# Performance work log

Hardware: AMD Instinct MI355X
Metric: run time of the kernel (lower is better)

The kernel has to match this reference:

```python
import jax, jax.numpy as jnp
import numpy as np

G, N, E, B, L, D, R, NB, H, LD = 5, 50000, 250000, 50, 200, 64, 5, 2, 4, 32
NU, NV = 100000, 50000
NE = NU + NV  # embedding rows


def _rgcn(x, src, dst, etype, basis, comp, root, bias):
    # basis-decomposed RGCN layer with per-(node,relation) mean aggregation
    xb = jnp.einsum('ni,bio->nbo', x, basis)              # [N,NB,out]
    msg = jnp.einsum('eb,ebo->eo', comp[etype], xb[src])  # [E,out]
    seg = dst * R + etype                                  # (node,relation) segment id
    agg = jax.ops.segment_sum(msg, seg, num_segments=N * R)
    cnt = jax.ops.segment_sum(jnp.ones_like(msg[:, 0]), seg, num_segments=N * R)
    agg = agg / jnp.maximum(cnt, 1.0)[:, None]
    return agg.reshape(N, R, -1).sum(1) + x @ root + bias


def _stam(inp, pos_emb, Qw, Kw, Vw, convW, convb):
    Bn = inp.shape[0]
    t = inp + pos_emb[None]                                # [2B,L,D]
    def heads(m):
        return (t @ m).reshape(Bn, L, H, D // H).transpose(0, 2, 1, 3)
    q, k, v = heads(Qw), heads(Kw), heads(Vw)
    scores = jnp.einsum('bhld,bhmd->bhlm', q, k) / np.float32(np.sqrt(L))
    att = jax.nn.softmax(scores, axis=-1)                  # mask is all-ones -> adder 0
    h = jnp.einsum('bhlm,bhmd->bhld', att, v).transpose(0, 2, 1, 3).reshape(Bn, L, D)
    ff = jnp.einsum('ol,bld->bod', convW, h) + convb[None, :, None] + h  # Conv1d k=1 over the L-channel axis + residual
    out = t + ff
    return out / jnp.maximum(jnp.linalg.norm(out, axis=2, keepdims=True), 1e-12)


def _forward(x, temporal_label, emb_table, basis0, comp0, root0, bias0,
             basisR, compR, rootR, biasR, pos_emb, Qw, Kw, Vw, convW, convb,
             aw1, ab1, aw2, mw1, mb1, mw2, mb2, l1w, l1b, l2w, l2b,
             edge_index, edge_type, centre_index, temporal_table):
    x_list, tem_list = [], []
    for g in range(G):
        xg = x[g]
        src, dst, et = edge_index[g, 0], edge_index[g, 1], edge_type[g]
        h = jnp.tanh(_rgcn(xg, src, dst, et, basis0, comp0, root0, bias0))
        states = [h]
        for l in range(3):
            h = jnp.tanh(_rgcn(h, src, dst, et, basisR[l], compR[l], rootR[l], biasR[l]))
            states.append(h)
        cs = jnp.concatenate(states, 1)                    # [N,128]
        u_idx = jnp.nonzero(xg[:, 0] == 1, size=B, fill_value=0)[0]
        i_idx = jnp.nonzero(xg[:, 1] == 1, size=B, fill_value=0)[0]
        x_list.append(jnp.concatenate([cs[u_idx], cs[i_idx]], 1))  # [B,256]
        tem_in = emb_table[temporal_table[g]]              # [2B,L,D]
        tem_out = _stam(tem_in, pos_emb, Qw, Kw, Vw, convW, convb)
        W1 = emb_table[centre_index[g]]                    # [2B,D]
        tw = jax.nn.softmax(jnp.einsum('btd,bd->bt', tem_out, W1), axis=1)
        am = tw * temporal_label[g]
        asum = am / jnp.sum(am, axis=1, keepdims=True)
        asum = jnp.where(jnp.isfinite(asum), asum, 0.0)
        _emb = jnp.einsum('bt,btd->bd', asum, tem_in)      # sparse mm equivalent
        tem_list.append(_emb.reshape(B, -1))               # [B,128]
    graph_tem = jnp.concatenate(tem_list, 1)               # [B,640]
    graph_emb = jnp.concatenate(x_list, 1)                 # [B,1280]
    sub = jnp.stack(x_list, 1)                             # [B,G,256]
    attK = jax.nn.relu(sub @ aw1 + ab1) @ aw2              # [B,G,1]
    attw = jax.nn.softmax(attK, axis=1)
    agg = jnp.sum(attw * sub, axis=1)                      # [B,256]
    meta = jax.nn.relu(agg @ mw1 + mb1) @ mw2 + mb2        # [B,1280]
    xcat = jnp.concatenate([meta * graph_emb, graph_tem], 1)  # [B,1920]
    hh = jax.nn.relu(xcat @ l1w + l1b)
    return (hh @ l2w + l2b)[:, 0]


def setup_inputs():
    key = jax.random.key(0)
    ks = jax.random.split(key, 32)
    cls = np.full((G, N), 2, dtype=np.int64)
    cls[:, :B] = 0          # users
    cls[:, B:2 * B] = 1     # items
    cls[:, 2 * B::2] = 3    # mix of 1-hop neighbor classes
    x = jax.nn.one_hot(jnp.asarray(cls), 4, dtype=jnp.float32)
    def nrm(k, shape, s=0.1):
        return jax.random.normal(k, shape, jnp.float32) * s
    return dict(
        x=x,
        edge_index=jax.random.randint(ks[0], (G, 2, E), 0, N),
        edge_type=jax.random.randint(ks[1], (G, E), 0, R),
        centre_index=jax.random.randint(ks[2], (G, 2 * B), 0, NE),
        temporal_table=jax.random.randint(ks[3], (G, 2 * B, L), 0, NE),
        temporal_label=(jax.random.uniform(ks[4], (G, 2 * B, L)) < 0.5).astype(jnp.float32),
        emb_table=nrm(ks[5], (NE, D), 0.01),
        basis0=nrm(ks[6], (NB, 4, LD)), comp0=nrm(ks[7], (R, NB), 1.0),
        root0=nrm(ks[8], (4, LD)), bias0=jnp.zeros((LD,), jnp.float32),
        basisR=nrm(ks[9], (3, NB, LD, LD)), compR=nrm(ks[10], (3, R, NB), 1.0),
        rootR=nrm(ks[11], (3, LD, LD)), biasR=jnp.zeros((3, LD), jnp.float32),
        pos_emb=nrm(ks[12], (L, D), 0.01),
        Qw=nrm(ks[13], (D, D), 0.01), Kw=nrm(ks[14], (D, D), 0.01), Vw=nrm(ks[15], (D, D), 0.01),
        convW=nrm(ks[16], (L, L), 0.05), convb=jnp.zeros((L,), jnp.float32),
        aw1=nrm(ks[17], (8 * LD, 8 * LD), 0.05), ab1=jnp.zeros((8 * LD,), jnp.float32),
        aw2=nrm(ks[18], (8 * LD, 1), 0.05),
        mw1=nrm(ks[19], (8 * LD, 16 * LD), 0.05), mb1=jnp.zeros((16 * LD,), jnp.float32),
        mw2=nrm(ks[20], (16 * LD, G * 8 * LD), 0.05), mb2=jnp.zeros((G * 8 * LD,), jnp.float32),
        l1w=nrm(ks[21], (G * 2 * D + G * 8 * LD, 128), 0.05), l1b=jnp.zeros((128,), jnp.float32),
        l2w=nrm(ks[22], (128, 1), 0.05), l2b=jnp.zeros((1,), jnp.float32),
    )


def reference(x, temporal_label, emb_table, basis0, comp0, root0, bias0,
              basisR, compR, rootR, biasR, pos_emb, Qw, Kw, Vw, convW, convb,
              aw1, ab1, aw2, mw1, mb1, mw2, mb2, l1w, l1b, l2w, l2b,
              edge_index, edge_type, centre_index, temporal_table):
    return _forward(x, temporal_label, emb_table, basis0, comp0, root0, bias0,
                    basisR, compR, rootR, biasR, pos_emb, Qw, Kw, Vw, convW, convb,
                    aw1, ab1, aw2, mw1, mb1, mw2, mb2, l1w, l1b, l2w, l2b,
                    edge_index, edge_type, centre_index, temporal_table)
```

## Files before the change

### kernel.cpp

```cpp
#include <hip/hip_runtime.h>
#include <hip/hip_bf16.h>

__global__ void IGMC_15247133901635_kernel() {}

#define cG 5
#define cN 50000
#define cE 250000
#define cB 50
#define cL 200
#define cD 64
#define cR 5
#define cNR 250000
#define cGB 500
#define NBLK 977

#define FP_UIDX   0
#define FP_BSUM   4096
#define FP_XLIST  28672
#define FP_EMBOUT 540672
#define FP_ATTK   668672
#define FP_METAH  672768
#define FP_XCAT   775168
#define FP_SAG    1159168
#define FP_INV    1559168
#define FP_CLS    2559168
#define FP_HA     3559168
#define FP_HB     9959168
#define FP_CUR    16359168
#define FP_OFF    21359168
#define FP_PERM   26359168
#define FP_INVC   31359168
#define FP_NEED   36359168ULL
#define FP2_MARK   36359168
#define FP2_LIST   37359168
#define FP2_CNT    38359168
#define FP2_COUNTS 38363264
#define FP2_NEED   38367360ULL

__global__ void k_prep(const float* xg, int* cls, int* cur) {
  int i = blockIdx.x * 256 + threadIdx.x;
  if (i < cNR) cur[i] = 0;
  if (i < cN) {
    int c = 0;
    if (xg[i * 4 + 1] == 1.0f) c = 1;
    else if (xg[i * 4 + 2] == 1.0f) c = 2;
    else if (xg[i * 4 + 3] == 1.0f) c = 3;
    cls[i] = c;
  }
}

__global__ void k_histg(const int* eid, const int* etg, int* cur) {
  int e = blockIdx.x * 256 + threadIdx.x;
  if (e < cE) atomicAdd(&cur[eid[e] * cR + etg[e]], 1);
}

__global__ void k_bsum(const int* cur, int* bsum) {
  __shared__ int sC[256];
  int t = threadIdx.x;
  int i = blockIdx.x * 256 + t;
  sC[t] = (i < cNR) ? cur[i] : 0;
  __syncthreads();
  for (int s = 128; s > 0; s >>= 1) {
    if (t < s) sC[t] += sC[t + s];
    __syncthreads();
  }
  if (t == 0) bsum[blockIdx.x] = sC[0];
}

__global__ void __launch_bounds__(1024) k_bscan(int* bsum) {
  __shared__ int sS[1024];
  int t = threadIdx.x;
  int v = (t < NBLK) ? bsum[t] : 0;
  sS[t] = v;
  __syncthreads();
  for (int off = 1; off < 1024; off <<= 1) {
    int add = (t >= off) ? sS[t - off] : 0;
    __syncthreads();
    sS[t] += add;
    __syncthreads();
  }
  if (t < NBLK) bsum[t] = sS[t] - v;
}

__global__ void k_mkoff(int* cur, int* off, const int* bbase) {
  __shared__ int sC[256];
  __shared__ int sO[256];
  int t = threadIdx.x;
  int i = blockIdx.x * 256 + t;
  int c = (i < cNR) ? cur[i] : 0;
  sC[t] = c;
  __syncthreads();
  if (t == 0) {
    int run = 0;
    for (int k = 0; k < 256; k++) { sO[k] = run; run += sC[k]; }
  }
  __syncthreads();
  if (i < cNR) {
    int v = bbase[blockIdx.x] + sO[t];
    off[i] = v;
    cur[i] = v;
  }
}

__global__ void k_scatter(const int* eis, const int* eid, const int* etg,
                          const int* cls, int* cur, int* perm) {
  int e = blockIdx.x * 256 + threadIdx.x;
  if (e >= cE) return;
  int src = eis[e];
  int r = etg[e];
  int bin = eid[e] * cR + r;
  int pos = atomicAdd(&cur[bin], 1);
  perm[pos] = src * 32 + r * 4 + cls[src];
}

__global__ void k_invc(const int* off, const int* cur, float* invc) {
  int i = blockIdx.x * 256 + threadIdx.x;
  if (i >= cNR) return;
  int st = off[i], en = cur[i];
  if (en > st) {
    float ic = 1.0f / (float)(en - st);
// ... 189 lines not shown
  for (; j + 1 < en; j += 2) {
    int p0 = perm[j], p1 = perm[j + 1];
    float i0 = invc[j], i1 = invc[j + 1];
    tot += sW0[(p0 & 31) * 32 + li] * i0 + sW0[(p1 & 31) * 32 + li] * i1;
  }
  if (j < en) tot += sW0[(perm[j] & 31) * 32 + li] * invc[j];
  float val = tanhf(tot + sRt[cls[n] * 32 + li] + sB[li]);
  hout[(long long)n * 32 + li] = val;
  if (inv) {
    int iv = inv[n];
    if (iv >= 0) xlist[iv + li] = val;
  }
}

__global__ void k_gatherR(const int* off, const int* cur, const int* perm,
                          const float* invc, const float* hin, const float* basis,
                          const float* comp, const float* root, const float* bias,
                          float* hout, const int* inv, float* xlist, int layer,
                          const int* list, const int* cntp) {
  int cnt = cN;
  if (cntp) {
    cnt = *cntp;
    if (blockIdx.x * 8 >= cnt) return;
  }
  __shared__ float sB0[1024];
  __shared__ float sB1[1024];
  __shared__ float sRt[1024];
  __shared__ float sZ0[8][32];
  __shared__ float sZ1[8][32];
  __shared__ float sHl[8][32];
  __shared__ float sBias[32];
  __shared__ float sC0[8];
  __shared__ float sC1[8];
  int t = threadIdx.x;
  for (int idx = t; idx < 1024; idx += 256) {
    sB0[idx] = basis[idx];
    sB1[idx] = basis[1024 + idx];
    sRt[idx] = root[idx];
  }
  if (t < 32) sBias[t] = bias[t];
  if (t < cR) { sC0[t] = comp[t * 2]; sC1[t] = comp[t * 2 + 1]; }
  __syncthreads();
  int nd = t >> 5, li = t & 31;
  int idx8 = blockIdx.x * 8 + nd;
  int n;
  if (list) n = (idx8 < cnt) ? list[idx8] : list[0];
  else n = idx8;
  sHl[nd][li] = hin[(long long)n * 32 + li];
  int st = off[n * 5], en = cur[n * 5 + 4];
  float z0 = 0.0f, z1 = 0.0f;
  int j = st;
  for (; j + 1 < en; j += 2) {
    int p0 = perm[j], p1 = perm[j + 1];
    float i0 = invc[j], i1 = invc[j + 1];
    float s0 = hin[(long long)(p0 >> 5) * 32 + li];
    float s1 = hin[(long long)(p1 >> 5) * 32 + li];
    int r0 = (p0 >> 2) & 7, r1 = (p1 >> 2) & 7;
    float w00 = sC0[r0] * i0, w10 = sC1[r0] * i0;
    float w01 = sC0[r1] * i1, w11 = sC1[r1] * i1;
    z0 += w00 * s0 + w01 * s1;
    z1 += w10 * s0 + w11 * s1;
  }
  if (j < en) {
    int p0 = perm[j];
    float i0 = invc[j];
    float s0 = hin[(long long)(p0 >> 5) * 32 + li];
    int r0 = (p0 >> 2) & 7;
    z0 += sC0[r0] * i0 * s0;
    z1 += sC1[r0] * i0 * s0;
  }
  sZ0[nd][li] = z0;
  sZ1[nd][li] = z1;
  __syncthreads();
  float a = sBias[li];
  for (int i = 0; i < 32; i++)
    a += sZ0[nd][i] * sB0[i * 32 + li] + sZ1[nd][i] * sB1[i * 32 + li] +
         sHl[nd][i] * sRt[i * 32 + li];
  float val = tanhf(a);
  hout[(long long)n * 32 + li] = val;
  if (inv) {
    int iv = inv[n];
    if (iv >= 0) xlist[iv + layer * 32 + li] = val;
  }
}

__global__ void k_uidx(const float* x, int* uidx) {
  int g = blockIdx.x >> 1, c = blockIdx.x & 1;
  __shared__ int sFlag[256];
  __shared__ int sBase;
  int t = threadIdx.x;
  if (t < cB) uidx[(g * 2 + c) * cB + t] = 0;
  if (t == 0) sBase = 0;
  __syncthreads();
  for (int chunk = 0; chunk < cN; chunk += 256) {
    int n = chunk + t;
    sFlag[t] = (n < cN && x[((long long)g * cN + n) * 4 + c] == 1.0f) ? 1 : 0;
    __syncthreads();
    if (t == 0) {
      int base = sBase;
      for (int t2 = 0; t2 < 256; t2++) {
        if (sFlag[t2]) {
          if (base < cB) uidx[(g * 2 + c) * cB + base] = chunk + t2;
          base++;
        }
      }
      sBase = base;
    }
    __syncthreads();
    if (sBase >= cB) break;
  }
}

__global__ void k_extract(const float* h, const int* uidx, float* xlist, int g, int layer) {
  int i = blockIdx.x * 256 + threadIdx.x;
  if (i >= 2 * cB * 32) return;
  int o = i & 31;
  int rest = i >> 5;
  int b = rest % cB, c = rest / cB;
  int node = uidx[(g * 2 + c) * cB + b];
  xlist[(g * cB + b) * 256 + c * 128 + layer * 32 + o] = h[(long long)node * 32 + o];
}

__global__ void k_attn2(const int* tt, const float* emb, const float* pos,
                        const float* Qw, const float* Kw, const float* Vw,
                        float* hatt, int gb_base) {
  int gbl = blockIdx.x >> 2, hh = blockIdx.x & 3;
  int gb = gb_base + gbl;
  __shared__ float smem[12160];
  float* sQ = smem;
  float* sK = smem + 3200;
  float* sV = smem + 6400;
  float* sT = smem + 9600;
  int t = threadIdx.x;
  float wreg[64];
  int c48 = t % 48, rgrp = t / 48;
  int mat = c48 >> 4, dh = c48 & 15;
  if (t < 192) {
    const float* W = (mat == 0) ? Qw : ((mat == 1) ? Kw : Vw);
    const float* wp = W + hh * 16 + dh;
#pragma unroll
    for (int i = 0; i < 64; i += 4) {
      wreg[i] = wp[i * 64];
      wreg[i + 1] = wp[(i + 1) * 64];
      wreg[i + 2] = wp[(i + 2) * 64];
      wreg[i + 3] = wp[(i + 3) * 64];
    }
  }
  const int* ttg = tt + (long long)gb * 200;
  float r[5];
#define LOADC(c)                                                        \
  {                                                                     \
    _Pragma("unroll")                                                   \
    for (int k = 0; k < 5; k++) {                                       \
      int idx = k * 256 + t;                                            \
      int row = idx >> 6, d2 = idx & 63;                                \
      int l = (c) * 20 + row;                                           \
      r[k] = emb[(long long)ttg[l] * 64 + d2] + pos[l * 64 + d2];       \
    }                                                                   \
  }
#define STOREC(pb)                                                      \
  {                                                                     \
    _Pragma("unroll")                                                   \
    for (int k = 0; k < 5; k++) sT[(pb) * 1280 + k * 256 + t] = r[k];   \
  }
  LOADC(0)
  STOREC(0)
// ... 131 lines not shown
  float w1 = emb[(long long)cen[gb] * 64 + d];
  __syncthreads();
  int o0 = og * 25;
  {
    const float* cwb = convW + o0 * 200;
    float acc[13];
#pragma unroll
    for (int q = 0; q < 13; q++) acc[q] = 0.0f;
    for (int l2 = 0; l2 < 200; l2 += 4) {
      float s0 = sH[(l2 + 0) * 64 + d];
      float s1 = sH[(l2 + 1) * 64 + d];
      float s2 = sH[(l2 + 2) * 64 + d];
      float s3 = sH[(l2 + 3) * 64 + d];
#pragma unroll
      for (int q = 0; q < 13; q++) {
        float4 c4 = *(const float4*)(cwb + q * 200 + l2);
        acc[q] += c4.x * s0 + c4.y * s1 + c4.z * s2 + c4.w * s3;
      }
    }
    float tv[13];
#pragma unroll
    for (int q = 0; q < 13; q++) {
      int o = o0 + q;
      tv[q] = emb[(long long)tt[(long long)gb * 200 + o] * 64 + d] + pos[o * 64 + d];
    }
#pragma unroll
    for (int q = 0; q < 13; q++) {
      int o = o0 + q;
      float outv = tv[q] + acc[q] + convb[o] + sH[o * 64 + d];
      float r1 = outv * outv;
      float r2 = outv * w1;
      for (int s = 32; s > 0; s >>= 1) {
        r1 += __shfl_xor(r1, s);
        r2 += __shfl_xor(r2, s);
      }
      if (d == 0) {
        float dn = sqrtf(r1);
        if (dn < 1e-12f) dn = 1e-12f;
        sAg[(long long)gb * 200 + o] = r2 / dn;
      }
    }
  }
  {
    const float* cwb = convW + (o0 + 13) * 200;
    float acc[12];
#pragma unroll
    for (int q = 0; q < 12; q++) acc[q] = 0.0f;
    for (int l2 = 0; l2 < 200; l2 += 4) {
      float s0 = sH[(l2 + 0) * 64 + d];
      float s1 = sH[(l2 + 1) * 64 + d];
      float s2 = sH[(l2 + 2) * 64 + d];
      float s3 = sH[(l2 + 3) * 64 + d];
#pragma unroll
      for (int q = 0; q < 12; q++) {
        float4 c4 = *(const float4*)(cwb + q * 200 + l2);
        acc[q] += c4.x * s0 + c4.y * s1 + c4.z * s2 + c4.w * s3;
      }
    }
    float tv[12];
#pragma unroll
    for (int q = 0; q < 12; q++) {
      int o = o0 + 13 + q;
      tv[q] = emb[(long long)tt[(long long)gb * 200 + o] * 64 + d] + pos[o * 64 + d];
    }
#pragma unroll
    for (int q = 0; q < 12; q++) {
      int o = o0 + 13 + q;
      float outv = tv[q] + acc[q] + convb[o] + sH[o * 64 + d];
      float r1 = outv * outv;
      float r2 = outv * w1;
      for (int s = 32; s > 0; s >>= 1) {
        r1 += __shfl_xor(r1, s);
        r2 += __shfl_xor(r2, s);
      }
      if (d == 0) {
        float dn = sqrtf(r1);
        if (dn < 1e-12f) dn = 1e-12f;
        sAg[(long long)gb * 200 + o] = r2 / dn;
      }
    }
  }
}

__global__ void k_tw(const float* sAg, const int* tt, const float* lab,
                     const float* emb, float* embout) {
  int gb = blockIdx.x;
  __shared__ float sA[200];
  __shared__ float sP[256];
  __shared__ float sR[256];
  int t = threadIdx.x;
  float a0 = (t < 200) ? sAg[(long long)gb * 200 + t] : -1e30f;
  sP[t] = a0;
  __syncthreads();
  for (int s = 128; s > 0; s >>= 1) {
    if (t < s) { float o2 = sP[t + s]; if (o2 > sP[t]) sP[t] = o2; }
    __syncthreads();
  }
  float mx = sP[0];
  __syncthreads();
  float a = 0.0f;
  if (t < 200) a = expf(a0 - mx) * lab[(long long)gb * 200 + t];
  sP[t] = a;
  __syncthreads();
  for (int s = 128; s > 0; s >>= 1) {
    if (t < s) sP[t] += sP[t + s];
    __syncthreads();
  }
  float sum = sP[0];
  __syncthreads();
  if (t < 200) sA[t] = (sum > 0.0f) ? a / sum : 0.0f;
  __syncthreads();
  int og = t >> 6, d = t & 63;
  float acc2 = 0.0f;
  for (int l = og * 50; l < og * 50 + 50; l++)
    acc2 += sA[l] * emb[(long long)tt[(long long)gb * 200 + l] * 64 + d];
  sR[t] = acc2;
  __syncthreads();
  if (t < 64)
    embout[(long long)gb * 64 + t] = sR[t] + sR[64 + t] + sR[128 + t] + sR[192 + t];
}

__global__ void k_att1(const float* xlist, const float* aw1, const float* ab1,
                       const float* aw2, float* attK) {
  int blk = blockIdx.x;
  int b = blk / cG, g = blk - b * cG;
  int j = threadIdx.x;
  __shared__ float sRed[256];
  const float* sub = xlist + (g * cB + b) * 256;
  float acc = ab1[j];
  for (int i = 0; i < 256; i++) acc += sub[i] * aw1[i * 256 + j];
  if (acc < 0.0f) acc = 0.0f;
  sRed[j] = acc * aw2[j];
  __syncthreads();
  for (int s = 128; s > 0; s >>= 1) {
    if (j < s) sRed[j] += sRed[j + s];
    __syncthreads();
  }
  if (j == 0) attK[b * cG + g] = sRed[0];
}

__global__ void k_hm(const float* attK, const float* xlist, const float* mw1,
                     const float* mb1, float* metah) {
  int b = blockIdx.x;
  __shared__ float sAgg[256];
  int t = threadIdx.x;
  float a0 = attK[b * 5 + 0], a1 = attK[b * 5 + 1], a2 = attK[b * 5 + 2],
        a3 = attK[b * 5 + 3], a4 = attK[b * 5 + 4];
  float mx = a0;
  if (a1 > mx) mx = a1;
  if (a2 > mx) mx = a2;
  if (a3 > mx) mx = a3;
  if (a4 > mx) mx = a4;
  float e0 = expf(a0 - mx), e1 = expf(a1 - mx), e2 = expf(a2 - mx),
        e3 = expf(a3 - mx), e4 = expf(a4 - mx);
  float s = e0 + e1 + e2 + e3 + e4;
  sAgg[t] = (e0 * xlist[(0 * cB + b) * 256 + t] + e1 * xlist[(1 * cB + b) * 256 + t] +
             e2 * xlist[(2 * cB + b) * 256 + t] + e3 * xlist[(3 * cB + b) * 256 + t] +
             e4 * xlist[(4 * cB + b) * 256 + t]) / s;
  __syncthreads();
  for (int j = t; j < 512; j += 256) {
    float acc = mb1[j];
    for (int i = 0; i < 256; i++) acc += sAgg[i] * mw1[i * 512 + j];
    if (acc < 0.0f) acc = 0.0f;
    metah[b * 512 + j] = acc;
  }
}

__global__ void k_m2(const float* metah, const float* mw2, const float* mb2,
                     const float* xlist, const float* embout, float* xcat) {
  int i = blockIdx.x * 256 + threadIdx.x;
  if (i >= cB * 1920) return;
  int b = i / 1920, j = i - b * 1920;
  if (j < 1280) {
    float acc = mb2[j];
    const float* mh = metah + b * 512;
    for (int k = 0; k < 512; k++) acc += mh[k] * mw2[k * 1280 + j];
    int g = j >> 8, jj = j & 255;
    xcat[b * 1920 + j] = acc * xlist[(g * cB + b) * 256 + jj];
  } else {
    int jj = j - 1280;
    int g = jj >> 7, r = jj & 127;
    xcat[b * 1920 + j] = embout[(g * 100 + 2 * b + (r >> 6)) * 64 + (r & 63)];
  }
}

__global__ void k_l12(const float* xcat, const float* l1w, const float* l1b,
                      const float* l2w, const float* l2b, float* out) {
  int b = blockIdx.x;
  int t = threadIdx.x;
  __shared__ float sHH[128];
  float acc = l1b[t];
  const float* xc = xcat + b * 1920;
  for (int i = 0; i < 1920; i++) acc += xc[i] * l1w[i * 128 + t];
  if (acc < 0.0f) acc = 0.0f;
  sHH[t] = acc * l2w[t];
  __syncthreads();
  for (int s = 64; s > 0; s >>= 1) {
    if (t < s) sHH[t] += sHH[t + s];
    __syncthreads();
  }
  if (t == 0) out[b] = sHH[0] + l2b[0];
}

extern "C" void kernel_launch(void* const* d_in, const int* in_sizes, int n_in,
                              void* d_out, int out_size, void* d_ws, size_t ws_size,
                              hipStream_t stream) {
  const float* x      = (const float*)d_in[0];
  const int* ei       = (const int*)d_in[1];
  const int* et       = (const int*)d_in[2];
  const int* cen      = (const int*)d_in[3];
  const int* tt       = (const int*)d_in[4];
  const float* lab    = (const float*)d_in[5];
  const float* emb    = (const float*)d_in[6];
  const float* basis0 = (const float*)d_in[7];
  const float* comp0  = (const float*)d_in[8];
  const float* root0  = (const float*)d_in[9];
  const float* bias0  = (const float*)d_in[10];
  const float* basisR = (const float*)d_in[11];
  const float* compR  = (const float*)d_in[12];
  const float* rootR  = (const float*)d_in[13];
  const float* biasR  = (const float*)d_in[14];
  const float* pos    = (const float*)d_in[15];
  const float* Qw     = (const float*)d_in[16];
  const float* Kw     = (const float*)d_in[17];
  const float* Vw     = (const float*)d_in[18];
  const float* convW  = (const float*)d_in[19];
  const float* convb  = (const float*)d_in[20];
  const float* aw1    = (const float*)d_in[21];
  const float* ab1    = (const float*)d_in[22];
  const float* aw2    = (const float*)d_in[23];
  const float* mw1    = (const float*)d_in[24];
  const float* mb1    = (const float*)d_in[25];
  const float* mw2    = (const float*)d_in[26];
  const float* mb2    = (const float*)d_in[27];
  const float* l1w    = (const float*)d_in[28];
  const float* l1b    = (const float*)d_in[29];
  const float* l2w    = (const float*)d_in[30];
  const float* l2b    = (const float*)d_in[31];
  float* out          = (float*)d_out;
  char* p = (char*)d_ws;
  (void)in_sizes; (void)n_in; (void)out_size;

  if (ws_size >= FP_NEED) {
    int*   uidx   = (int*)(p + FP_UIDX);
    int*   bsumA  = (int*)(p + FP_BSUM);
    float* xlist  = (float*)(p + FP_XLIST);
    float* embout = (float*)(p + FP_EMBOUT);
    float* attK   = (float*)(p + FP_ATTK);
    float* metah  = (float*)(p + FP_METAH);
    float* xcat   = (float*)(p + FP_XCAT);
    float* sAg    = (float*)(p + FP_SAG);
    int*   inv    = (int*)(p + FP_INV);
    int*   clsA   = (int*)(p + FP_CLS);
    float* h_a    = (float*)(p + FP_HA);
    float* h_b    = (float*)(p + FP_HB);
    int*   curA   = (int*)(p + FP_CUR);
    int*   offA   = (int*)(p + FP_OFF);
    int*   permA  = (int*)(p + FP_PERM);
    float* invcA  = (float*)(p + FP_INVC);
    float* hatt   = h_a;

    bool pruned = (ws_size >= FP2_NEED);
    int* markA  = pruned ? (int*)(p + FP2_MARK) : nullptr;
    int* listA  = pruned ? (int*)(p + FP2_LIST) : nullptr;
    int* cntA   = pruned ? (int*)(p + FP2_CNT) : nullptr;
    int* counts = pruned ? (int*)(p + FP2_COUNTS) : nullptr;

    k_invinit<<<NBLK, 256, 0, stream>>>(inv);
    k_uidx<<<cG * 2, 256, 0, stream>>>(x, uidx);
    k_mkinv<<<1, 512, 0, stream>>>(uidx, inv);

    k_prepB<<<cG * NBLK, 256, 0, stream>>>(x, clsA, curA, markA);
    k_histgB<<<cG * NBLK, 256, 0, stream>>>(ei, et, curA);
    k_bsumB<<<cG * NBLK, 256, 0, stream>>>(curA, bsumA);
    k_bscanB<<<cG, 1024, 0, stream>>>(bsumA);
    k_mkoffB<<<cG * NBLK, 256, 0, stream>>>(curA, offA, bsumA, invcA);
    k_scatterB<<<cG * NBLK, 256, 0, stream>>>(ei, et, clsA, curA, permA);

    if (pruned) {
      k_mark<<<cG, 128, 0, stream>>>(uidx, markA, listA, cntA, counts);
      for (int k = 1; k <= 3; k++) {
        k_expand<<<cG * EXB, 256, 0, stream>>>(offA, curA, permA, markA, listA,
                                               cntA, counts, k);
        k_snap<<<1, 64, 0, stream>>>(counts, cntA, k);
      }
    }

    for (int g = 0; g < cG; g++) {
      const int*   offg  = offA + (long long)g * cNR;
      const int*   curg  = curA + (long long)g * cNR;
      const int*   permg = permA + (long long)g * cE;
      const float* invcg = invcA + (long long)g * cE;
      const int*   clsg  = clsA + (long long)g * cN;
      const int*   invg  = inv + (long long)g * cN;
      const int*   listg = pruned ? (listA + (long long)g * cN) : nullptr;
      const int* c0 = pruned ? (counts + g * 4 + 3) : nullptr;
      k_gather0<<<6250, 256, 0, stream>>>(offg, curg, permg, invcg, clsg, basis0,
                                          comp0, root0, bias0, h_b, invg, xlist,
                                          listg, c0);
      float* hin = h_b;
      float* hou = h_a;
      for (int l = 0; l < 3; l++) {
        const int* cl = pruned ? (counts + g * 4 + (2 - l)) : nullptr;
        k_gatherR<<<6250, 256, 0, stream>>>(offg, curg, permg, invcg, hin,
                                            basisR + l * 2048, compR + l * 10,
                                            rootR + l * 1024, biasR + l * 32, hou,
                                            invg, xlist, l + 1, listg, cl);
        float* tmp = hin; hin = hou; hou = tmp;
      }
    }

    k_attn2<<<2000, 256, 0, stream>>>(tt, emb, pos, Qw, Kw, Vw, hatt, 0);
    k_conv<<<500, 512, 0, stream>>>(hatt, tt, cen, emb, pos, convW, convb, sAg, 0);
    k_tw<<<500, 256, 0, stream>>>(sAg, tt, lab, emb, embout);

    k_att1<<<cB * cG, 256, 0, stream>>>(xlist, aw1, ab1, aw2, attK);
    k_hm<<<cB, 256, 0, stream>>>(attK, xlist, mw1, mb1, metah);
    k_m2<<<375, 256, 0, stream>>>(metah, mw2, mb2, xlist, embout, xcat);
    k_l12<<<cB, 128, 0, stream>>>(xcat, l1w, l1b, l2w, l2b, out);
    return;
  }

  int*   uidx   = (int*)(p);
  int*   clsb   = (int*)(p + 4096);
  int*   cur    = (int*)(p + 208896);
  int*   off    = (int*)(p + 1212416);
  int*   perm   = (int*)(p + 2215936);
  float* invc   = (float*)(p + 3219456);
  int*   bsum   = (int*)(p + 4222976);
  float* xlist  = (float*)(p + 4227072);
  float* embout = (float*)(p + 4741120);
  float* attK   = (float*)(p + 4870144);
  float* metah  = (float*)(p + 4874240);
  float* xcat   = (float*)(p + 4980736);
  char*  arena  = p + 5368832;
  float* h_a    = (float*)(arena);
  float* h_b    = (float*)(arena + 6400000);
  float* hatt   = (float*)(arena);
  float* sAg    = (float*)(p + 4874240);

  k_uidx<<<cG * 2, 256, 0, stream>>>(x, uidx);

  for (int g = 0; g < cG; g++) {
    const int* eis = ei + (long long)g * 2 * cE;
    const int* eid = eis + cE;
    const int* etg = et + (long long)g * cE;
    const float* xg = x + (long long)g * cN * 4;
    k_prep<<<NBLK, 256, 0, stream>>>(xg, clsb, cur);
    k_histg<<<NBLK, 256, 0, stream>>>(eid, etg, cur);
    k_bsum<<<NBLK, 256, 0, stream>>>(cur, bsum);
    k_bscan<<<1, 1024, 0, stream>>>(bsum);
    k_mkoff<<<NBLK, 256, 0, stream>>>(cur, off, bsum);
    k_scatter<<<NBLK, 256, 0, stream>>>(eis, eid, etg, clsb, cur, perm);
    k_invc<<<NBLK, 256, 0, stream>>>(off, cur, invc);
    k_gather0<<<6250, 256, 0, stream>>>(off, cur, perm, invc, clsb, basis0, comp0,
                                        root0, bias0, h_b, nullptr, nullptr,
                                        nullptr, nullptr);
    k_extract<<<13, 256, 0, stream>>>(h_b, uidx, xlist, g, 0);
    float* hin = h_b;
    float* hou = h_a;
    for (int l = 0; l < 3; l++) {
      k_gatherR<<<6250, 256, 0, stream>>>(off, cur, perm, invc, hin,
                                          basisR + l * 2048, compR + l * 10,
                                          rootR + l * 1024, biasR + l * 32, hou,
                                          nullptr, nullptr, 0, nullptr, nullptr);
      k_extract<<<13, 256, 0, stream>>>(hou, uidx, xlist, g, l + 1);
      float* tmp = hin; hin = hou; hou = tmp;
    }
  }

  for (int c = 0; c < 2; c++) {
    k_attn2<<<1000, 256, 0, stream>>>(tt, emb, pos, Qw, Kw, Vw, hatt, c * 250);
    k_conv<<<250, 512, 0, stream>>>(hatt, tt, cen, emb, pos, convW, convb, sAg,
                                    c * 250);
  }
  k_tw<<<500, 256, 0, stream>>>(sAg, tt, lab, emb, embout);

  k_att1<<<cB * cG, 256, 0, stream>>>(xlist, aw1, ab1, aw2, attK);
  k_hm<<<cB, 256, 0, stream>>>(attK, xlist, mw1, mb1, metah);
  k_m2<<<375, 256, 0, stream>>>(metah, mw2, mb2, xlist, embout, xcat);
  k_l12<<<cB, 128, 0, stream>>>(xcat, l1w, l1b, l2w, l2b, out);
}
```

Before: 950.3 us.

## Fuse conv+temporal-weighting and the four head kernels into single kernels

Merges the Conv1d/normalise kernel with the temporal softmax-weighting kernel so attention scores stay in shared memory, and collapses att1, hm, m2 and l12 into one per-sample head kernel. This removes four launches and several global round trips for small intermediates. In exchange, the head now runs on only 50 blocks, and each block serially does the five attention MLPs and the full mw2 matvec, so there is much less parallelism than the 250- and 375-block kernels it replaces.

```diff
diff --git a/kernel.cpp b/kernel.cpp
--- a/kernel.cpp
+++ b/kernel.cpp
@@ -688,6 +688,136 @@
   }
 }
 
+__global__ void __launch_bounds__(512, 4) k_convtw(
+    const float* hatt, const int* tt, const int* cen,
+    const float* emb, const float* pos, const float* convW,
+    const float* convb, const float* lab, float* embout, int gb_base) {
+  int gbl = blockIdx.x;
+  int gb = gb_base + gbl;
+  __shared__ float sH[12800];
+  __shared__ float sA[200];
+  float* sP = sH;
+  float* sR = sH + 256;
+  int t = threadIdx.x;
+  const float4* hb4 = (const float4*)(hatt + (long long)gbl * 12800);
+  float4* sH4 = (float4*)sH;
+  for (int i = t; i < 3200; i += 512) sH4[i] = hb4[i];
+  int og = t >> 6, d = t & 63;
+  float w1 = emb[(long long)cen[gb] * 64 + d];
+  __syncthreads();
+  int o0 = og * 25;
+  {
+    const float* cwb = convW + o0 * 200;
+    float acc[13];
+#pragma unroll
+    for (int q = 0; q < 13; q++) acc[q] = 0.0f;
+    for (int l2 = 0; l2 < 200; l2 += 4) {
+      float s0 = sH[(l2 + 0) * 64 + d];
+      float s1 = sH[(l2 + 1) * 64 + d];
+      float s2 = sH[(l2 + 2) * 64 + d];
+      float s3 = sH[(l2 + 3) * 64 + d];
+#pragma unroll
+      for (int q = 0; q < 13; q++) {
+        float4 c4 = *(const float4*)(cwb + q * 200 + l2);
+        acc[q] += c4.x * s0 + c4.y * s1 + c4.z * s2 + c4.w * s3;
+      }
+    }
+    float tv[13];
+#pragma unroll
+    for (int q = 0; q < 13; q++) {
+      int o = o0 + q;
+      tv[q] = emb[(long long)tt[(long long)gb * 200 + o] * 64 + d] + pos[o * 64 + d];
+    }
+#pragma unroll
+    for (int q = 0; q < 13; q++) {
+      int o = o0 + q;
+      float outv = tv[q] + acc[q] + convb[o] + sH[o * 64 + d];
+      float r1 = outv * outv;
+      float r2 = outv * w1;
+      for (int s = 32; s > 0; s >>= 1) {
+        r1 += __shfl_xor(r1, s);
+        r2 += __shfl_xor(r2, s);
+      }
+      if (d == 0) {
+        float dn = sqrtf(r1);
+        if (dn < 1e-12f) dn = 1e-12f;
+        sA[o] = r2 / dn;
+      }
+    }
+  }
+  {
+    const float* cwb = convW + (o0 + 13) * 200;
+    float acc[12];
+#pragma unroll
+    for (int q = 0; q < 12; q++) acc[q] = 0.0f;
+    for (int l2 = 0; l2 < 200; l2 += 4) {
+      float s0 = sH[(l2 + 0) * 64 + d];
+      float s1 = sH[(l2 + 1) * 64 + d];
+      float s2 = sH[(l2 + 2) * 64 + d];
+      float s3 = sH[(l2 + 3) * 64 + d];
+#pragma unroll
+      for (int q = 0; q < 12; q++) {
+        float4 c4 = *(const float4*)(cwb + q * 200 + l2);
+        acc[q] += c4.x * s0 + c4.y * s1 + c4.z * s2 + c4.w * s3;
+      }
+    }
+    float tv[12];
+#pragma unroll
+    for (int q = 0; q < 12; q++) {
+      int o = o0 + 13 + q;
+      tv[q] = emb[(long long)tt[(long long)gb * 200 + o] * 64 + d] + pos[o * 64 + d];
+    }
+#pragma unroll
+    for (int q = 0; q < 12; q++) {
+      int o = o0 + 13 + q;
+      float outv = tv[q] + acc[q] + convb[o] + sH[o * 64 + d];
+      float r1 = outv * outv;
+      float r2 = outv * w1;
+      for (int s = 32; s > 0; s >>= 1) {
+        r1 += __shfl_xor(r1, s);
+        r2 += __shfl_xor(r2, s);
+      }
+      if (d == 0) {
+        float dn = sqrtf(r1);
+        if (dn < 1e-12f) dn = 1e-12f;
+        sA[o] = r2 / dn;
+      }
+    }
+  }
+  __syncthreads();
+  float a0 = (t < 200) ? sA[t] : -1e30f;
+  if (t < 256) sP[t] = a0;
+  __syncthreads();
+  for (int s = 128; s > 0; s >>= 1) {
+    if (t < s) { float o2 = sP[t + s]; if (o2 > sP[t]) sP[t] = o2; }
+    __syncthreads();
+  }
+  float mx = sP[0];
+  __syncthreads();
+  float a = 0.0f;
+  if (t < 200) a = expf(a0 - mx) * lab[(long long)gb * 200 + t];
+  if (t < 256) sP[t] = a;
+  __syncthreads();
+  for (int s = 128; s > 0; s >>= 1) {
+    if (t < s) sP[t] += sP[t + s];
+    __syncthreads();
+  }
+  float sum = sP[0];
+  __syncthreads();
+  if (t < 200) sA[t] = (sum > 0.0f) ? a / sum : 0.0f;
+  __syncthreads();
+  if (t < 256) {
+    float acc2 = 0.0f;
+    int og2 = t >> 6, d2 = t & 63;
+    for (int l = og2 * 50; l < og2 * 50 + 50; l++)
+      acc2 += sA[l] * emb[(long long)tt[(long long)gb * 200 + l] * 64 + d2];
+    sR[t] = acc2;
+  }
+  __syncthreads();
+  if (t < 64)
+    embout[(long long)gb * 64 + t] = sR[t] + sR[64 + t] + sR[128 + t] + sR[192 + t];
+}
+
 __global__ void k_tw(const float* sAg, const int* tt, const float* lab,
                      const float* emb, float* embout) {
   int gb = blockIdx.x;
@@ -800,6 +930,82 @@
   for (int i = 0; i < 1920; i++) acc += xc[i] * l1w[i * 128 + t];
   if (acc < 0.0f) acc = 0.0f;
   sHH[t] = acc * l2w[t];
+  __syncthreads();
+  for (int s = 64; s > 0; s >>= 1) {
+    if (t < s) sHH[t] += sHH[t + s];
+    __syncthreads();
+  }
+  if (t == 0) out[b] = sHH[0] + l2b[0];
+}
+
+__global__ void k_head(const float* xlist, const float* aw1, const float* ab1,
+                       const float* aw2, const float* mw1, const float* mb1,
+                       const float* mw2, const float* mb2, const float* embout,
+                       const float* l1w, const float* l1b, const float* l2w,
+                       const float* l2b, float* out) {
+  int b = blockIdx.x;
+  __shared__ float sRed[256];
+  __shared__ float sK5[5];
+  __shared__ float sAgg[256];
+  __shared__ float sMh[512];
+  __shared__ float sXc[1920];
+  __shared__ float sHH[128];
+  int t = threadIdx.x;
+  for (int g = 0; g < cG; g++) {
+    const float* sub = xlist + (g * cB + b) * 256;
+    float acc = ab1[t];
+    for (int i = 0; i < 256; i++) acc += sub[i] * aw1[i * 256 + t];
+    if (acc < 0.0f) acc = 0.0f;
+    sRed[t] = acc * aw2[t];
+    __syncthreads();
+    for (int s = 128; s > 0; s >>= 1) {
+      if (t < s) sRed[t] += sRed[t + s];
+      __syncthreads();
+    }
+    if (t == 0) sK5[g] = sRed[0];
+    __syncthreads();
+  }
+  {
+    float a0 = sK5[0], a1 = sK5[1], a2 = sK5[2], a3 = sK5[3], a4 = sK5[4];
+    float mx = a0;
+    if (a1 > mx) mx = a1;
+    if (a2 > mx) mx = a2;
+    if (a3 > mx) mx = a3;
+    if (a4 > mx) mx = a4;
+    float e0 = expf(a0 - mx), e1 = expf(a1 - mx), e2 = expf(a2 - mx),
+          e3 = expf(a3 - mx), e4 = expf(a4 - mx);
+    float s = e0 + e1 + e2 + e3 + e4;
+    sAgg[t] = (e0 * xlist[(0 * cB + b) * 256 + t] + e1 * xlist[(1 * cB + b) * 256 + t] +
+               e2 * xlist[(2 * cB + b) * 256 + t] + e3 * xlist[(3 * cB + b) * 256 + t] +
+               e4 * xlist[(4 * cB + b) * 256 + t]) / s;
+    __syncthreads();
+    for (int j = t; j < 512; j += 256) {
+      float acc = mb1[j];
+      for (int i = 0; i < 256; i++) acc += sAgg[i] * mw1[i * 512 + j];
+      if (acc < 0.0f) acc = 0.0f;
+      sMh[j] = acc;
+    }
+    __syncthreads();
+  }
+  for (int j = t; j < 1920; j += 256) {
+    if (j < 1280) {
+      float acc = mb2[j];
+      for (int k = 0; k < 512; k++) acc += sMh[k] * mw2[k * 1280 + j];
+      int g = j >> 8, jj = j & 255;
+      sXc[j] = acc * xlist[(g * cB + b) * 256 + jj];
+    } else {
+      int jj = j - 1280;
+      int g = jj >> 7, r = jj & 127;
+      sXc[j] = embout[(g * 100 + 2 * b + (r >> 6)) * 64 + (r & 63)];
+    }
+  }
+  __syncthreads();
+  if (t < 128) {
+    float acc = l1b[t];
+    for (int i = 0; i < 1920; i++) acc += sXc[i] * l1w[i * 128 + t];
+    if (acc < 0.0f) acc = 0.0f;
+    sHH[t] = acc * l2w[t];
+  }
   __syncthreads();
   for (int s = 64; s > 0; s >>= 1) {
     if (t < s) sHH[t] += sHH[t + s];
@@ -852,10 +1058,6 @@
     int*   bsumA  = (int*)(p + FP_BSUM);
     float* xlist  = (float*)(p + FP_XLIST);
     float* embout = (float*)(p + FP_EMBOUT);
-    float* attK   = (float*)(p + FP_ATTK);
-    float* metah  = (float*)(p + FP_METAH);
-    float* xcat   = (float*)(p + FP_XCAT);
-    float* sAg    = (float*)(p + FP_SAG);
     int*   inv    = (int*)(p + FP_INV);
     int*   clsA   = (int*)(p + FP_CLS);
     float* h_a    = (float*)(p + FP_HA);
@@ -917,13 +1119,10 @@
     }
 
     k_attn2<<<2000, 256, 0, stream>>>(tt, emb, pos, Qw, Kw, Vw, hatt, 0);
-    k_conv<<<500, 512, 0, stream>>>(hatt, tt, cen, emb, pos, convW, convb, sAg, 0);
-    k_tw<<<500, 256, 0, stream>>>(sAg, tt, lab, emb, embout);
-
-    k_att1<<<cB * cG, 256, 0, stream>>>(xlist, aw1, ab1, aw2, attK);
-    k_hm<<<cB, 256, 0, stream>>>(attK, xlist, mw1, mb1, metah);
-    k_m2<<<375, 256, 0, stream>>>(metah, mw2, mb2, xlist, embout, xcat);
-    k_l12<<<cB, 128, 0, stream>>>(xcat, l1w, l1b, l2w, l2b, out);
+    k_convtw<<<500, 512, 0, stream>>>(hatt, tt, cen, emb, pos, convW, convb,
+                                      lab, embout, 0);
+    k_head<<<cB, 256, 0, stream>>>(xlist, aw1, ab1, aw2, mw1, mb1, mw2, mb2,
+                                   embout, l1w, l1b, l2w, l2b, out);
     return;
   }
 
```

New measurement: 1.080 ms. 13.7% more time.

## Batch pruned RGCN gather kernels across all five graphs in one launch

Applied to the files above, without the earlier changes.

Adds batched variants of the layer-0 and layer-R gather kernels that cover all five graphs in a single grid, each with its own per-graph hidden-state buffer. This replaces twenty small launches, most of whose blocks exit early under pruning, with four large ones. The aim is to cut launch overhead and tail idle time, at the cost of a larger workspace (about 102 MB). If the workspace is smaller, the code falls back to the per-graph loop.

```diff
diff --git a/kernel.cpp b/kernel.cpp
--- a/kernel.cpp
+++ b/kernel.cpp
@@ -13,6 +13,7 @@
 #define cNR 250000
 #define cGB 500
 #define NBLK 977
+#define GB0 6250
 
 #define FP_UIDX   0
 #define FP_BSUM   4096
@@ -36,6 +37,9 @@
 #define FP2_CNT    38359168
 #define FP2_COUNTS 38363264
 #define FP2_NEED   38367360ULL
+#define FP3_HA     38367360
+#define FP3_HB     70367360
+#define FP3_NEED   102367360ULL
 
 __global__ void k_prep(const float* xg, int* cls, int* cur) {
   int i = blockIdx.x * 256 + threadIdx.x;
@@ -391,6 +395,128 @@
     int iv = inv[n];
     if (iv >= 0) xlist[iv + layer * 32 + li] = val;
   }
+}
+
+__global__ void k_gather0B(const int* offA, const int* curA, const int* permA,
+                           const float* invcA, const int* clsA,
+                           const float* basis0, const float* comp0,
+                           const float* root0, const float* bias0,
+                           float* houtB, const int* inv, float* xlist,
+                           const int* listA, const int* counts) {
+  int g = blockIdx.x / GB0;
+  int b2 = blockIdx.x - g * GB0;
+  int cnt = counts[g * 4 + 3];
+  if (b2 * 8 >= cnt) return;
+  const int* off = offA + (long long)g * cNR;
+  const int* cur = curA + (long long)g * cNR;
+  const int* perm = permA + (long long)g * cE;
+  const float* invc = invcA + (long long)g * cE;
+  const int* cls = clsA + (long long)g * cN;
+  const int* list = listA + (long long)g * cN;
+  const int* invg = inv + (long long)g * cN;
+  float* hout = houtB + (long long)g * cN * 32;
+  __shared__ float sW0[640];
+  __shared__ float sRt[128];
+  __shared__ float sB[32];
+  int t = threadIdx.x;
+  for (int idx = t; idx < 640; idx += 256) {
+    int r = idx / 128, rem = idx - r * 128;
+    sW0[idx] = comp0[r * 2] * basis0[rem] + comp0[r * 2 + 1] * basis0[128 + rem];
+  }
+  if (t < 128) sRt[t] = root0[t];
+  if (t < 32) sB[t] = bias0[t];
+  __syncthreads();
+  int nd = t >> 5, li = t & 31;
+  int idx8 = b2 * 8 + nd;
+  int n = (idx8 < cnt) ? list[idx8] : list[0];
+  int st = off[n * 5], en = cur[n * 5 + 4];
+  float tot = 0.0f;
+  int j = st;
+  for (; j + 1 < en; j += 2) {
+    int p0 = perm[j], p1 = perm[j + 1];
+    float i0 = invc[j], i1 = invc[j + 1];
+    tot += sW0[(p0 & 31) * 32 + li] * i0 + sW0[(p1 & 31) * 32 + li] * i1;
+  }
+  if (j < en) tot += sW0[(perm[j] & 31) * 32 + li] * invc[j];
+  float val = tanhf(tot + sRt[cls[n] * 32 + li] + sB[li]);
+  hout[(long long)n * 32 + li] = val;
+  int iv = invg[n];
+  if (iv >= 0) xlist[iv + li] = val;
+}
+
+__global__ void k_gatherRB(const int* offA, const int* curA, const int* permA,
+                           const float* invcA, const float* hinB,
+                           const float* basis, const float* comp,
+                           const float* root, const float* bias,
+                           float* houtB, const int* inv, float* xlist, int layer,
+                           const int* listA, const int* counts, int koff) {
+  int g = blockIdx.x / GB0;
+  int b2 = blockIdx.x - g * GB0;
+  int cnt = counts[g * 4 + koff];
+  if (b2 * 8 >= cnt) return;
+  const int* off = offA + (long long)g * cNR;
+  const int* cur = curA + (long long)g * cNR;
+  const int* perm = permA + (long long)g * cE;
+  const float* invc = invcA + (long long)g * cE;
+  const int* list = listA + (long long)g * cN;
+  const int* invg = inv + (long long)g * cN;
+  const float* hin = hinB + (long long)g * cN * 32;
+  float* hout = houtB + (long long)g * cN * 32;
+  __shared__ float sB0[1024];
+  __shared__ float sB1[1024];
+  __shared__ float sRt[1024];
+  __shared__ float sZ0[8][32];
+  __shared__ float sZ1[8][32];
+  __shared__ float sHl[8][32];
+  __shared__ float sBias[32];
+  __shared__ float sC0[8];
+  __shared__ float sC1[8];
+  int t = threadIdx.x;
+  for (int idx = t; idx < 1024; idx += 256) {
+    sB0[idx] = basis[idx];
+    sB1[idx] = basis[1024 + idx];
+    sRt[idx] = root[idx];
+  }
+  if (t < 32) sBias[t] = bias[t];
+  if (t < cR) { sC0[t] = comp[t * 2]; sC1[t] = comp[t * 2 + 1]; }
+  __syncthreads();
+  int nd = t >> 5, li = t & 31;
+  int idx8 = b2 * 8 + nd;
+  int n = (idx8 < cnt) ? list[idx8] : list[0];
+  sHl[nd][li] = hin[(long long)n * 32 + li];
+  int st = off[n * 5], en = cur[n * 5 + 4];
+  float z0 = 0.0f, z1 = 0.0f;
+  int j = st;
+  for (; j + 1 < en; j += 2) {
+    int p0 = perm[j], p1 = perm[j + 1];
+    float i0 = invc[j], i1 = invc[j + 1];
+    float s0 = hin[(long long)(p0 >> 5) * 32 + li];
+    float s1 = hin[(long long)(p1 >> 5) * 32 + li];
+    int r0 = (p0 >> 2) & 7, r1 = (p1 >> 2) & 7;
+    float w00 = sC0[r0] * i0, w10 = sC1[r0] * i0;
+    float w01 = sC0[r1] * i1, w11 = sC1[r1] * i1;
+    z0 += w00 * s0 + w01 * s1;
+    z1 += w10 * s0 + w11 * s1;
+  }
+  if (j < en) {
+    int p0 = perm[j];
+    float i0 = invc[j];
+    float s0 = hin[(long long)(p0 >> 5) * 32 + li];
+    int r0 = (p0 >> 2) & 7;
+    z0 += sC0[r0] * i0 * s0;
+    z1 += sC1[r0] * i0 * s0;
+  }
+  sZ0[nd][li] = z0;
+  sZ1[nd][li] = z1;
+  __syncthreads();
+  float a = sBias[li];
+  for (int i = 0; i < 32; i++)
+    a += sZ0[nd][i] * sB0[i * 32 + li] + sZ1[nd][i] * sB1[i * 32 + li] +
+         sHl[nd][i] * sRt[i * 32 + li];
+  float val = tanhf(a);
+  hout[(long long)n * 32 + li] = val;
+  int iv = invg[n];
+  if (iv >= 0) xlist[iv + layer * 32 + li] = val;
 }
 
 __global__ void k_uidx(const float* x, int* uidx) {
@@ -864,13 +990,16 @@
     int*   offA   = (int*)(p + FP_OFF);
     int*   permA  = (int*)(p + FP_PERM);
     float* invcA  = (float*)(p + FP_INVC);
-    float* hatt   = h_a;
-
-    bool pruned = (ws_size >= FP2_NEED);
+
+    bool pruned  = (ws_size >= FP2_NEED);
+    bool batched = (ws_size >= FP3_NEED);
     int* markA  = pruned ? (int*)(p + FP2_MARK) : nullptr;
     int* listA  = pruned ? (int*)(p + FP2_LIST) : nullptr;
     int* cntA   = pruned ? (int*)(p + FP2_CNT) : nullptr;
     int* counts = pruned ? (int*)(p + FP2_COUNTS) : nullptr;
+    float* hA5  = batched ? (float*)(p + FP3_HA) : nullptr;
+    float* hB5  = batched ? (float*)(p + FP3_HB) : nullptr;
+    float* hatt = batched ? hA5 : h_a;
 
     k_invinit<<<NBLK, 256, 0, stream>>>(inv);
     k_uidx<<<cG * 2, 256, 0, stream>>>(x, uidx);
@@ -892,27 +1021,43 @@
       }
     }
 
-    for (int g = 0; g < cG; g++) {
-      const int*   offg  = offA + (long long)g * cNR;
-      const int*   curg  = curA + (long long)g * cNR;
-      const int*   permg = permA + (long long)g * cE;
-      const float* invcg = invcA + (long long)g * cE;
-      const int*   clsg  = clsA + (long long)g * cN;
-      const int*   invg  = inv + (long long)g * cN;
-      const int*   listg = pruned ? (listA + (long long)g * cN) : nullptr;
-      const int* c0 = pruned ? (counts + g * 4 + 3) : nullptr;
-      k_gather0<<<6250, 256, 0, stream>>>(offg, curg, permg, invcg, clsg, basis0,
-                                          comp0, root0, bias0, h_b, invg, xlist,
-                                          listg, c0);
-      float* hin = h_b;
-      float* hou = h_a;
+    if (batched) {
+      k_gather0B<<<cG * GB0, 256, 0, stream>>>(offA, curA, permA, invcA, clsA,
+                                               basis0, comp0, root0, bias0, hB5,
+                                               inv, xlist, listA, counts);
+      float* hinB = hB5;
+      float* houB = hA5;
       for (int l = 0; l < 3; l++) {
-        const int* cl = pruned ? (counts + g * 4 + (2 - l)) : nullptr;
-        k_gatherR<<<6250, 256, 0, stream>>>(offg, curg, permg, invcg, hin,
-                                            basisR + l * 2048, compR + l * 10,
-                                            rootR + l * 1024, biasR + l * 32, hou,
-                                            invg, xlist, l + 1, listg, cl);
-        float* tmp = hin; hin = hou; hou = tmp;
+        k_gatherRB<<<cG * GB0, 256, 0, stream>>>(offA, curA, permA, invcA, hinB,
+                                                 basisR + l * 2048, compR + l * 10,
+                                                 rootR + l * 1024, biasR + l * 32,
+                                                 houB, inv, xlist, l + 1, listA,
+                                                 counts, 2 - l);
+        float* tmp = hinB; hinB = houB; houB = tmp;
+      }
+    } else {
+      for (int g = 0; g < cG; g++) {
+        const int*   offg  = offA + (long long)g * cNR;
+        const int*   curg  = curA + (long long)g * cNR;
+        const int*   permg = permA + (long long)g * cE;
+        const float* invcg = invcA + (long long)g * cE;
+        const int*   clsg  = clsA + (long long)g * cN;
+        const int*   invg  = inv + (long long)g * cN;
+        const int*   listg = pruned ? (listA + (long long)g * cN) : nullptr;
+        const int* c0 = pruned ? (counts + g * 4 + 3) : nullptr;
+        k_gather0<<<GB0, 256, 0, stream>>>(offg, curg, permg, invcg, clsg, basis0,
+                                           comp0, root0, bias0, h_b, invg, xlist,
+                                           listg, c0);
+        float* hin = h_b;
+        float* hou = h_a;
+        for (int l = 0; l < 3; l++) {
+          const int* cl = pruned ? (counts + g * 4 + (2 - l)) : nullptr;
+          k_gatherR<<<GB0, 256, 0, stream>>>(offg, curg, permg, invcg, hin,
+                                             basisR + l * 2048, compR + l * 10,
+                                             rootR + l * 1024, biasR + l * 32, hou,
+                                             invg, xlist, l + 1, listg, cl);
+          float* tmp = hin; hin = hou; hou = tmp;
+        }
       }
     }
 
@@ -959,17 +1104,17 @@
     k_mkoff<<<NBLK, 256, 0, stream>>>(cur, off, bsum);
     k_scatter<<<NBLK, 256, 0, stream>>>(eis, eid, etg, clsb, cur, perm);
     k_invc<<<NBLK, 256, 0, stream>>>(off, cur, invc);
-    k_gather0<<<6250, 256, 0, stream>>>(off, cur, perm, invc, clsb, basis0, comp0,
-                                        root0, bias0, h_b, nullptr, nullptr,
-                                        nullptr, nullptr);
+    k_gather0<<<GB0, 256, 0, stream>>>(off, cur, perm, invc, clsb, basis0, comp0,
+                                       root0, bias0, h_b, nullptr, nullptr,
+                                       nullptr, nullptr);
     k_extract<<<13, 256, 0, stream>>>(h_b, uidx, xlist, g, 0);
     float* hin = h_b;
     float* hou = h_a;
     for (int l = 0; l < 3; l++) {
-      k_gatherR<<<6250, 256, 0, stream>>>(off, cur, perm, invc, hin,
-                                          basisR + l * 2048, compR + l * 10,
-                                          rootR + l * 1024, biasR + l * 32, hou,
-                                          nullptr, nullptr, 0, nullptr, nullptr);
+      k_gatherR<<<GB0, 256, 0, stream>>>(off, cur, perm, invc, hin,
+                                         basisR + l * 2048, compR + l * 10,
+                                         rootR + l * 1024, biasR + l * 32, hou,
+                                         nullptr, nullptr, 0, nullptr, nullptr);
       k_extract<<<13, 256, 0, stream>>>(hou, uidx, xlist, g, l + 1);
       float* tmp = hin; hin = hou; hou = tmp;
     }
```

New measurement: 884.9 us. 1.07x faster.
